# Performance work log

Measured on AMD Instinct MI355X. Metric: run time of the kernel, lower is better.

## Reference

```python
import jax, jax.numpy as jnp
import numpy as np
import math

E = 2048        # embed_dim
H = 16          # num_heads
HD = E // H // 2  # head_dim = 64
DEPTH = 12
LAMBDA_INIT = 0.8 - 0.6 * math.exp(-0.3 * DEPTH)


def setup_inputs() -> dict:
    key = jax.random.key(0)
    ks = jax.random.split(key, 9)
    s = 0.02
    return {
        "x": jax.random.normal(ks[0], (2, 2048, E), jnp.float32),
        "Wq": jax.random.normal(ks[1], (E, E), jnp.float32) * s,
        "Wk": jax.random.normal(ks[2], (E, E), jnp.float32) * s,  # n_rep = 1
        "Wv": jax.random.normal(ks[3], (E, E), jnp.float32) * s,
        "Wo": jax.random.normal(ks[4], (E, E), jnp.float32) * s,
        "lq1": jax.random.normal(ks[5], (HD,), jnp.float32) * 0.1,
        "lk1": jax.random.normal(ks[6], (HD,), jnp.float32) * 0.1,
        "lq2": jax.random.normal(ks[7], (HD,), jnp.float32) * 0.1,
        "lk2": jax.random.normal(ks[8], (HD,), jnp.float32) * 0.1,
    }


def reference(x, Wq, Wk, Wv, Wo, lq1, lk1, lq2, lk2):
    b, t, e = x.shape
    scaling = HD ** (-0.5)
    # projections; split into 2*H sub-heads of dim HD for q/k, H heads of 2*HD for v
    q = (x @ Wq).reshape(b, t, 2 * H, HD).transpose(0, 2, 1, 3) * scaling  # [b,2H,t,hd]
    k = (x @ Wk).reshape(b, t, 2 * H, HD).transpose(0, 2, 1, 3)           # [b,2H,t,hd]
    v = (x @ Wv).reshape(b, t, H, 2 * HD).transpose(0, 2, 1, 3)           # [b,H,t,2hd]

    scores = jnp.einsum('bhqd,bhkd->bhqk', q, k)  # [b,2H,t,t]
    causal = jnp.triu(jnp.full((t, t), -jnp.inf, dtype=jnp.float32), 1)
    aw = jax.nn.softmax((scores + causal).astype(jnp.float32), axis=-1)

    lam = (jnp.exp(jnp.sum(lq1 * lk1)) - jnp.exp(jnp.sum(lq2 * lk2)) + LAMBDA_INIT)
    aw = aw.reshape(b, H, 2, t, t)
    aw = aw[:, :, 0] - lam * aw[:, :, 1]  # differential attention

    attn = jnp.einsum('bhqk,bhkd->bhqd', aw, v)  # [b,H,t,2hd]
    # RMSNorm over last dim (no affine), eps=1e-5
    attn = attn * jax.lax.rsqrt(jnp.mean(attn * attn, axis=-1, keepdims=True) + 1e-5)
    attn = attn * (1.0 - LAMBDA_INIT)
    attn = attn.transpose(0, 2, 1, 3).reshape(b, t, H * 2 * HD)
    return attn @ Wo
```

## Files before the change

kernel.cpp:

```cpp
#include <hip/hip_runtime.h>
#include <stdint.h>

typedef __bf16 bf16_t;
typedef __bf16 bf16x8 __attribute__((ext_vector_type(8)));
typedef __bf16 bf16x4 __attribute__((ext_vector_type(4)));
typedef float  f32x4  __attribute__((ext_vector_type(4)));
typedef float  f32x16 __attribute__((ext_vector_type(16)));
typedef unsigned int u32;

#define L2E 1.44269504088896340736f
#define LAMBDA_INIT 0.7836057665316245f
#define ONE_MINUS_LAMBDA_INIT 0.2163942334683755f

__device__ __forceinline__ void gload_lds16(const void* g, void* l) {
  __builtin_amdgcn_global_load_lds(
      (const __attribute__((address_space(1))) char*)(uintptr_t)g,
      (__attribute__((address_space(3))) char*)(uintptr_t)l, 16, 0, 0);
}

__device__ __forceinline__ f32x4 mfma_bf16(bf16x8 a, bf16x8 b, f32x4 c) {
  return __builtin_amdgcn_mfma_f32_16x16x32_bf16(a, b, c, 0, 0, 0);
}
__device__ __forceinline__ f32x16 mfma32(bf16x8 a, bf16x8 b, f32x16 c) {
  return __builtin_amdgcn_mfma_f32_32x32x16_bf16(a, b, c, 0, 0, 0);
}

__device__ __forceinline__ u32 pkbf(float a, float b) {
  union { bf16_t h[2]; u32 u; } x;
  x.h[0] = (bf16_t)a; x.h[1] = (bf16_t)b;
  return x.u;
}
__device__ __forceinline__ void pl32swap(u32& a, u32& b) {
  asm volatile("v_permlane32_swap_b32 %0, %1" : "+v"(a), "+v"(b));
}

__global__ __launch_bounds__(256) void cvt_bf16(const float* __restrict__ in,
                                                bf16_t* __restrict__ out) {
  const size_t idx = ((size_t)blockIdx.x * 256 + threadIdx.x) * 8;
  float4 a = *(const float4*)(in + idx);
  float4 c = *(const float4*)(in + idx + 4);
  bf16x8 v;
  v[0] = (bf16_t)a.x; v[1] = (bf16_t)a.y; v[2] = (bf16_t)a.z; v[3] = (bf16_t)a.w;
  v[4] = (bf16_t)c.x; v[5] = (bf16_t)c.y; v[6] = (bf16_t)c.z; v[7] = (bf16_t)c.w;
  *(bf16x8*)(out + idx) = v;
}

struct WArgs {
  const float* W[4];
  bf16_t* WT[4];
  float sc[4];
};

__global__ __launch_bounds__(256) void cvt_wT_all(WArgs a) {
  __shared__ float t[64][65];
  const int i = blockIdx.z;
  const float* W = a.W[i];
  bf16_t* WT = a.WT[i];
  const float scale = a.sc[i];
  const int k0 = blockIdx.x * 64, n0 = blockIdx.y * 64;
  const int r = threadIdx.x >> 2, cg = threadIdx.x & 3;
#pragma unroll
  for (int q = 0; q < 4; ++q) {
    float4 v = *(const float4*)(W + (size_t)(k0 + r) * 2048 + n0 + cg * 16 + q * 4);
    t[r][cg * 16 + q * 4 + 0] = v.x;
    t[r][cg * 16 + q * 4 + 1] = v.y;
    t[r][cg * 16 + q * 4 + 2] = v.z;
    t[r][cg * 16 + q * 4 + 3] = v.w;
  }
  __syncthreads();
  bf16x8 o0, o1;
#pragma unroll
  for (int j = 0; j < 8; ++j) o0[j] = (bf16_t)(t[cg * 16 + j][r] * scale);
#pragma unroll
  for (int j = 0; j < 8; ++j) o1[j] = (bf16_t)(t[cg * 16 + 8 + j][r] * scale);
  bf16_t* dst = WT + (size_t)(n0 + r) * 2048 + k0 + cg * 16;
  *(bf16x8*)dst = o0;
  *(bf16x8*)(dst + 8) = o1;
}

__global__ void lam_kernel(const float* lq1, const float* lk1,
                           const float* lq2, const float* lk2, float* out) {
  const int l = threadIdx.x;
  float p1 = lq1[l] * lk1[l];
  float p2 = lq2[l] * lk2[l];
#pragma unroll
  for (int d = 1; d < 64; d <<= 1) {
    p1 += __shfl_xor(p1, d);
    p2 += __shfl_xor(p2, d);
  }
  if (l == 0) *out = expf(p1) - expf(p2) + LAMBDA_INIT;
}

__global__ __launch_bounds__(512, 2) void gemm256(const bf16_t* __restrict__ A,
                                                  const bf16_t* __restrict__ Bt,
                                                  bf16_t* __restrict__ Cqk) {
  extern __shared__ __align__(16) char sm[];
  const int tid = threadIdx.x;
  const int w = tid >> 6, lane = tid & 63;
  const int wr = w >> 2, wc = w & 3;
  const int lm = lane >> 4, ln = lane & 15;
  const int nwg = (int)(gridDim.x * gridDim.y);
  const int flat = (int)blockIdx.y * (int)gridDim.x + (int)blockIdx.x;
  const int swz = (flat & 7) * (nwg >> 3) + (flat >> 3);
  const int m0 = (swz & 15) * 256, n0 = (swz >> 4) * 256;

  int aoff[8], boff[4];
#pragma unroll
  for (int m = 0; m < 8; ++m) {
    const int row = wr * 128 + m * 16 + ln;
    aoff[m] = row * 64 + ((lm * 16) ^ ((((row >> 2) ^ row) & 3) << 4));
  }
#pragma unroll
  for (int n = 0; n < 4; ++n) {
    const int row = wc * 64 + n * 16 + ln;
    boff[n] = row * 64 + ((lm * 16) ^ ((((row >> 2) ^ row) & 3) << 4));
  }

  const bf16_t* gsrc[4];
  int ldst[4];
#pragma unroll
  for (int j = 0; j < 4; ++j) {
    const int r2 = j & 1, opB = j >> 1;
    const int row = r2 * 128 + w * 16 + (lane >> 2);
    const int colb = (lane & 3) * 16;
    const int cb = colb ^ ((((row >> 2) ^ row) & 3) << 4);
    gsrc[j] = (opB ? Bt + (size_t)(n0 + row) * 2048
                   : A + (size_t)(m0 + row) * 2048) + (cb >> 1);
    ldst[j] = opB * 16384 + r2 * 8192 + w * 1024;
  }

  const f32x4 vzero = {0.f, 0.f, 0.f, 0.f};
  f32x4 acc[8][4];
#pragma unroll
  for (int m = 0; m < 8; ++m)
#pragma unroll
    for (int n = 0; n < 4; ++n) acc[m][n] = vzero;

#pragma unroll
  for (int kt = 0; kt < 3; ++kt)
#pragma unroll
    for (int j = 0; j < 4; ++j)
      gload_lds16(gsrc[j] + kt * 32, sm + kt * 32768 + ldst[j]);
  asm volatile("s_waitcnt vmcnt(8)" ::: "memory");
  __builtin_amdgcn_s_barrier();

  for (int kt = 0; kt < 64; ++kt) {
    const char* sa = sm + (kt & 3) * 32768;
    const char* sb = sa + 16384;
    const int stage = kt + 3;
    char* sd = sm + (stage & 3) * 32768;
    bf16x8 bfr[4], af[4];

#pragma unroll
    for (int n = 0; n < 4; ++n) bfr[n] = *(const bf16x8*)(sb + boff[n]);
#pragma unroll
    for (int m = 0; m < 4; ++m) af[m] = *(const bf16x8*)(sa + aoff[m]);
    if (stage < 64) {
      gload_lds16(gsrc[0] + stage * 32, sd + ldst[0]);
      gload_lds16(gsrc[1] + stage * 32, sd + ldst[1]);
    }
    __builtin_amdgcn_s_barrier();
    __builtin_amdgcn_s_setprio(1);
#pragma unroll
    for (int m = 0; m < 4; ++m)
#pragma unroll
      for (int n = 0; n < 4; ++n) acc[m][n] = mfma_bf16(af[m], bfr[n], acc[m][n]);
    __builtin_amdgcn_s_setprio(0);
    __builtin_amdgcn_s_barrier();

#pragma unroll
    for (int m = 0; m < 4; ++m) af[m] = *(const bf16x8*)(sa + aoff[4 + m]);
    if (stage < 64) {
      gload_lds16(gsrc[2] + stage * 32, sd + ldst[2]);
      gload_lds16(gsrc[3] + stage * 32, sd + ldst[3]);
    }
    __builtin_amdgcn_s_barrier();
    __builtin_amdgcn_s_setprio(1);
#pragma unroll
    for (int m = 0; m < 4; ++m)
#pragma unroll
      for (int n = 0; n < 4; ++n)
        acc[4 + m][n] = mfma_bf16(af[m], bfr[n], acc[4 + m][n]);
    __builtin_amdgcn_s_setprio(0);
    if (kt < 61) {
      asm volatile("s_waitcnt vmcnt(8)" ::: "memory");
    } else if (kt == 61) {
      asm volatile("s_waitcnt vmcnt(4)" ::: "memory");
    } else if (kt == 62) {
      asm volatile("s_waitcnt vmcnt(0)" ::: "memory");
    }
    __builtin_amdgcn_s_barrier();
  }

  bf16_t* C = Cqk + (size_t)(n0 >> 11) * (4096u * 2048u);
#pragma unroll
  for (int m = 0; m < 8; ++m)
#pragma unroll
    for (int n = 0; n < 4; ++n)
#pragma unroll
      for (int r = 0; r < 4; ++r) {
        const size_t grow = m0 + wr * 128 + m * 16 + lm * 4 + r;
        const int gcol = (n0 + wc * 64 + n * 16 + ln) & 2047;
        C[grow * 2048 + gcol] = (bf16_t)acc[m][n][r];
      }
}

template <int OUTMODE>
__global__ __launch_bounds__(256, 2) void gemm_bt(const bf16_t* __restrict__ A,
                                                  const bf16_t* __restrict__ Bt,
                                                  void* __restrict__ Cv) {
  __shared__ __align__(16) bf16_t As[128 * 64];
  __shared__ __align__(16) bf16_t Bs[128 * 64];
  const int tid = threadIdx.x;
  const int w = tid >> 6, lane = tid & 63;
  const int wr = w >> 1, wc = w & 1;
  const int lm = lane >> 4, ln = lane & 15;
  const int nwg = (int)(gridDim.x * gridDim.y);
  const int flat = (int)blockIdx.y * (int)gridDim.x + (int)blockIdx.x;
  const int swz = (flat & 7) * (nwg >> 3) + (flat >> 3);
  const int m0 = (swz & 31) * 128, n0 = (swz >> 5) * 128;

  const f32x4 vzero = {0.f, 0.f, 0.f, 0.f};
  f32x4 acc[4][4];
#pragma unroll
  for (int m = 0; m < 4; ++m)
#pragma unroll
    for (int n = 0; n < 4; ++n) acc[m][n] = vzero;

  for (int k0 = 0; k0 < 2048; k0 += 64) {
    __syncthreads();
#pragma unroll
    for (int j = 0; j < 4; ++j) {
      const int inst = w * 4 + j;
      const int row = inst * 8 + (lane >> 3);
      const int cb = ((lane & 7) * 16) ^ ((row & 7) << 4);
      gload_lds16(A + (size_t)(m0 + row) * 2048 + k0 + (cb >> 1),
                  (char*)As + inst * 1024);
      gload_lds16(Bt + (size_t)(n0 + row) * 2048 + k0 + (cb >> 1),
                  (char*)Bs + inst * 1024);
    }
    asm volatile("s_waitcnt vmcnt(0)" ::: "memory");
    __syncthreads();

#pragma unroll
    for (int kc = 0; kc < 2; ++kc) {
      bf16x8 af[4], bfr[4];
#pragma unroll
      for (int m = 0; m < 4; ++m) {
        const int row = wr * 64 + m * 16 + ln;
        int off = row * 128 + kc * 64 + lm * 16;
        off ^= (row & 7) << 4;
        af[m] = *(const bf16x8*)((const char*)As + off);
      }
#pragma unroll
      for (int n = 0; n < 4; ++n) {
        const int row = wc * 64 + n * 16 + ln;
        int off = row * 128 + kc * 64 + lm * 16;
        off ^= (row & 7) << 4;
        bfr[n] = *(const bf16x8*)((const char*)Bs + off);
      }
      __builtin_amdgcn_s_setprio(1);
#pragma unroll
      for (int m = 0; m < 4; ++m)
#pragma unroll
        for (int n = 0; n < 4; ++n) acc[m][n] = mfma_bf16(af[m], bfr[n], acc[m][n]);
      __builtin_amdgcn_s_setprio(0);
    }
  }

  if (OUTMODE == 1) {
    bf16_t* C = (bf16_t*)Cv;
#pragma unroll
    for (int m = 0; m < 4; ++m) {
      const int growb = m0 + wr * 64 + m * 16 + lm * 4;
      const int bb = growb >> 11, t = growb & 2047;
      const int kt = t >> 6, kk = (t >> 4) & 3, hi2 = (t >> 3) & 1, e0 = t & 7;
#pragma unroll
      for (int n = 0; n < 4; ++n) {
        const int gcol = n0 + wc * 64 + n * 16 + ln;
        const int hh = gcol >> 7, g = (gcol >> 5) & 3, l31o = gcol & 31;
        bf16x4 v;
#pragma unroll
        for (int r = 0; r < 4; ++r) v[r] = (bf16_t)acc[m][n][r];
        const size_t idx = ((size_t)((bb * 16 + hh) * 32 + kt)) * 8192 +
                           (size_t)(((g * 4 + kk) * 64 + hi2 * 32 + l31o) * 8 + e0);
        *(bf16x4*)(C + idx) = v;
      }
    }
  } else {
    float* C = (float*)Cv;
#pragma unroll
    for (int m = 0; m < 4; ++m)
#pragma unroll
      for (int n = 0; n < 4; ++n)
#pragma unroll
        for (int r = 0; r < 4; ++r) {
          const size_t grow = m0 + wr * 64 + m * 16 + lm * 4 + r;
          const int gcol = n0 + wc * 64 + n * 16 + ln;
          C[grow * 2048 + gcol] = acc[m][n][r];
        }
  }
}

__global__ __launch_bounds__(256, 2) void flash_diff(const bf16_t* __restrict__ Q,
                                                     const bf16_t* __restrict__ K,
                                                     const bf16_t* __restrict__ Vf,
                                                     bf16_t* __restrict__ attnb,
                                                     const float* __restrict__ lamP) {
  __shared__ __align__(16) char smem[32768];

  const int tid = threadIdx.x;
  const int w = tid >> 6, lane = tid & 63;
  const int qh = w >> 1, s = w & 1;
  const int l31 = lane & 31, hi = lane >> 5;

  const int bid = (int)blockIdx.x;
  const int xcd = bid & 7, p = bid >> 3;
  const int qtp = p & 15, g2 = p >> 4;
  const int hb = g2 * 8 + xcd;
  const int h = hb & 15, b = hb >> 4;
  const size_t bt0 = (size_t)b * 2048;
  const float lam = *lamP;

  auto stage_k = [&](int buf, int k0) {
#pragma unroll
    for (int j = 0; j < 4; ++j) {
      const int inst = w * 4 + j;
      const int row = inst * 4 + (lane >> 4);
      const int cb = ((lane & 15) * 16) ^ ((row & 15) << 4);
      gload_lds16(K + (bt0 + k0 + row) * 2048 + h * 128 + (cb >> 1),
                  smem + buf * 16384 + inst * 1024);
    }
  };

  for (int half = 0; half < 2; ++half) {
    const int qt = half == 0 ? qtp : 31 - qtp;
    const int q0 = qt * 64;
    const int qloc = qh * 32 + l31;

    bf16x8 qf[4];
#pragma unroll
    for (int kc = 0; kc < 4; ++kc)
      qf[kc] = *(const bf16x8*)(Q + (bt0 + q0 + qloc) * 2048 + h * 128 +
                                s * 64 + kc * 16 + hi * 8);

    stage_k(0, 0);
    asm volatile("s_waitcnt vmcnt(0)" ::: "memory");
    __syncthreads();

    f32x16 accv[4];
#pragma unroll
    for (int m = 0; m < 4; ++m)
#pragma unroll
      for (int r = 0; r < 16; ++r) accv[m][r] = 0.f;
    float lsum = 0.f;

    int cur = 0;
    for (int kt = 0; kt <= qt; ++kt) {
      if (kt < qt) stage_k(cur ^ 1, (kt + 1) * 64);
      const char* Ksb = (const char*)smem + cur * 16384;

      const char* vsrc = (const char*)Vf +
                         (((size_t)((b * 16 + h) * 32 + kt)) << 14) + lane * 16;

      bf16x8 pf[2][2];
#pragma unroll
      for (int mt = 0; mt < 2; ++mt) {
        f32x16 sa;
#pragma unroll
        for (int r = 0; r < 16; ++r) sa[r] = 0.f;
        const int row = mt * 32 + l31;
        const int rswz = (row & 15) << 4;
        __builtin_amdgcn_s_setprio(1);
#pragma unroll
        for (int kc = 0; kc < 4; ++kc) {
          int off = row * 256 + s * 128 + kc * 32 + hi * 16;
          off ^= rswz;
          bf16x8 kf = *(const bf16x8*)(Ksb + off);
          sa = mfma32(kf, qf[kc], sa);
        }
        __builtin_amdgcn_s_setprio(0);

        if (kt == qt) {
#pragma unroll
          for (int r = 0; r < 16; ++r) {
            const int key = mt * 32 + (r & 3) + 8 * (r >> 2) + 4 * hi;
            if (key > qloc) sa[r] = -1e30f;
          }
        }
        float pv[16];
#pragma unroll
        for (int r = 0; r < 16; ++r) {
          pv[r] = exp2f(sa[r]);
          lsum += pv[r];
        }
        u32 c0 = pkbf(pv[0], pv[1]),   c1 = pkbf(pv[2], pv[3]);
        u32 c2 = pkbf(pv[4], pv[5]),   c3 = pkbf(pv[6], pv[7]);
        u32 c4 = pkbf(pv[8], pv[9]),   c5 = pkbf(pv[10], pv[11]);
        u32 c6 = pkbf(pv[12], pv[13]), c7 = pkbf(pv[14], pv[15]);
        pl32swap(c0, c2); pl32swap(c1, c3);
        pl32swap(c4, c6); pl32swap(c5, c7);
        union { u32 u[4]; bf16x8 v; } f0, f1;
        f0.u[0] = c0; f0.u[1] = c1; f0.u[2] = c2; f0.u[3] = c3;
        f1.u[0] = c4; f1.u[1] = c5; f1.u[2] = c6; f1.u[3] = c7;
        pf[mt][0] = f0.v;
        pf[mt][1] = f1.v;
      }

#pragma unroll
      for (int g = 0; g < 4; ++g) {
        bf16x8 vf[4];
#pragma unroll
        for (int kk = 0; kk < 4; ++kk)
          vf[kk] = *(const bf16x8*)(vsrc + (g * 4 + kk) * 1024);
        __builtin_amdgcn_s_setprio(1);
#pragma unroll
        for (int kk = 0; kk < 4; ++kk)
          accv[g] = mfma32(vf[kk], pf[kk >> 1][kk & 1], accv[g]);
        __builtin_amdgcn_s_setprio(0);
      }

      asm volatile("s_waitcnt vmcnt(0)" ::: "memory");
      __syncthreads();
      cur ^= 1;
    }

    lsum += __shfl_xor(lsum, 32);
    const float rl = 1.0f / lsum;
    float* Obuf = (float*)smem;

    if (s == 1) {
#pragma unroll
      for (int mt4 = 0; mt4 < 4; ++mt4)
#pragma unroll
        for (int q2 = 0; q2 < 4; ++q2) {
          f32x4 v;
#pragma unroll
          for (int e = 0; e < 4; ++e) v[e] = accv[mt4][q2 * 4 + e] * rl;
          const int d = mt4 * 32 + q2 * 8 + hi * 4;
          *(f32x4*)(Obuf + (size_t)qloc * 128 + d) = v;
        }
    }
    __syncthreads();
    if (s == 0) {
      float o[4][16];
      float ss = 0.f;
#pragma unroll
      for (int mt4 = 0; mt4 < 4; ++mt4)
#pragma unroll
        for (int q2 = 0; q2 < 4; ++q2) {
          const int d = mt4 * 32 + q2 * 8 + hi * 4;
          f32x4 ov = *(const f32x4*)(Obuf + (size_t)qloc * 128 + d);
#pragma unroll
          for (int e = 0; e < 4; ++e) {
            const float v = accv[mt4][q2 * 4 + e] * rl - lam * ov[e];
            o[mt4][q2 * 4 + e] = v;
            ss += v * v;
          }
        }
      ss += __shfl_xor(ss, 32);
      const float sc = rsqrtf(ss * (1.0f / 128.f) + 1e-5f) * ONE_MINUS_LAMBDA_INIT;
      const size_t grow = bt0 + q0 + qloc;
#pragma unroll
      for (int mt4 = 0; mt4 < 4; ++mt4)
#pragma unroll
        for (int q2 = 0; q2 < 4; ++q2) {
          const int d = mt4 * 32 + q2 * 8 + hi * 4;
          bf16x4 v;
#pragma unroll
          for (int e = 0; e < 4; ++e) v[e] = (bf16_t)(o[mt4][q2 * 4 + e] * sc);
          *(bf16x4*)(attnb + grow * 2048 + h * 128 + d) = v;
        }
    }
    __syncthreads();
  }
}

extern "C" void kernel_launch(void* const* d_in, const int* in_sizes, int n_in,
                              void* d_out, int out_size, void* d_ws, size_t ws_size,
                              hipStream_t stream) {
  const float* x   = (const float*)d_in[0];
  const float* Wq  = (const float*)d_in[1];
  const float* Wk  = (const float*)d_in[2];
  const float* Wv  = (const float*)d_in[3];
  const float* Wo  = (const float*)d_in[4];
  const float* lq1 = (const float*)d_in[5];
  const float* lk1 = (const float*)d_in[6];
  const float* lq2 = (const float*)d_in[7];
  const float* lk2 = (const float*)d_in[8];

  char* ws = (char*)d_ws;
  bf16_t* xb    = (bf16_t*)(ws + 0);
  bf16_t* wqT   = (bf16_t*)(ws + 16777216);
  bf16_t* wvT   = (bf16_t*)(ws + 33554432);
  bf16_t* woT   = (bf16_t*)(ws + 41943040);
  bf16_t* Qb    = (bf16_t*)(ws + 50331648);
  bf16_t* Kb    = (bf16_t*)(ws + 67108864);
  bf16_t* Vfb   = (bf16_t*)(ws + 16777216);
  bf16_t* attnb = (bf16_t*)(ws + 0);
  float*  lamP  = (float*)(ws + 83886080);

  hipFuncSetAttribute((const void*)gemm256,
                      hipFuncAttributeMaxDynamicSharedMemorySize, 131072);

  cvt_bf16<<<4096, 256, 0, stream>>>(x, xb);
  WArgs wa;
  wa.W[0] = Wq; wa.W[1] = Wk; wa.W[2] = Wv; wa.W[3] = Wo;
  wa.WT[0] = wqT; wa.WT[1] = wqT + 4194304; wa.WT[2] = wvT; wa.WT[3] = woT;
  wa.sc[0] = 0.125f * L2E; wa.sc[1] = 1.0f; wa.sc[2] = 1.0f; wa.sc[3] = 1.0f;
  cvt_wT_all<<<dim3(32, 32, 4), 256, 0, stream>>>(wa);
  lam_kernel<<<1, 64, 0, stream>>>(lq1, lk1, lq2, lk2, lamP);

  gemm256<<<dim3(16, 16), 512, 131072, stream>>>(xb, wqT, Qb);
  gemm_bt<1><<<dim3(32, 16), 256, 0, stream>>>(xb, wvT, (void*)Vfb);

  flash_diff<<<512, 256, 0, stream>>>(Qb, Kb, Vfb, attnb, lamP);

  gemm_bt<2><<<dim3(32, 16), 256, 0, stream>>>(attnb, woT, d_out);
}
```

Before: 272.4 us.

## Split flash attention KV loop across two wave groups with LDS merge

Doubles the flash_diff block to 512 threads and has two wave groups process the even and odd key tiles in parallel. Each group stages its own K tiles into separate LDS halves, and partial accumulators and row sums are merged through shared memory before the differential combine and RMSNorm. This shortens the serial KV loop per block to raise parallelism in the causal attention. In exchange it doubles LDS to 64KB and adds an extra reduction pass with syncs, which may lower occupancy, and waves with no tile on short rows sit idle.

```diff
diff --git a/kernel.cpp b/kernel.cpp
--- a/kernel.cpp
+++ b/kernel.cpp
@@ -302,16 +302,18 @@
   }
 }
 
-__global__ __launch_bounds__(256, 2) void flash_diff(const bf16_t* __restrict__ Q,
+__global__ __launch_bounds__(512, 2) void flash_diff(const bf16_t* __restrict__ Q,
                                                      const bf16_t* __restrict__ K,
                                                      const bf16_t* __restrict__ Vf,
                                                      bf16_t* __restrict__ attnb,
                                                      const float* __restrict__ lamP) {
-  __shared__ __align__(16) char smem[32768];
+  __shared__ __align__(16) char smem[65536];
+  __shared__ float lsumb[2][64];
 
   const int tid = threadIdx.x;
   const int w = tid >> 6, lane = tid & 63;
-  const int qh = w >> 1, s = w & 1;
+  const int kh = w & 1, s = (w >> 1) & 1, qh = w >> 2;
+  const int wg = w >> 1;
   const int l31 = lane & 31, hi = lane >> 5;
 
   const int bid = (int)blockIdx.x;
@@ -322,14 +324,19 @@
   const size_t bt0 = (size_t)b * 2048;
   const float lam = *lamP;
 
+  f32x16 vz16;
+#pragma unroll
+  for (int r = 0; r < 16; ++r) vz16[r] = 0.f;
+  asm volatile("" : "+v"(vz16));
+
   auto stage_k = [&](int buf, int k0) {
 #pragma unroll
     for (int j = 0; j < 4; ++j) {
-      const int inst = w * 4 + j;
+      const int inst = wg * 4 + j;
       const int row = inst * 4 + (lane >> 4);
       const int cb = ((lane & 15) * 16) ^ ((row & 15) << 4);
       gload_lds16(K + (bt0 + k0 + row) * 2048 + h * 128 + (cb >> 1),
-                  smem + buf * 16384 + inst * 1024);
+                  smem + kh * 32768 + buf * 16384 + inst * 1024);
     }
   };
 
@@ -344,80 +351,81 @@
       qf[kc] = *(const bf16x8*)(Q + (bt0 + q0 + qloc) * 2048 + h * 128 +
                                 s * 64 + kc * 16 + hi * 8);
 
-    stage_k(0, 0);
+    if (kh <= qt) stage_k(0, kh * 64);
     asm volatile("s_waitcnt vmcnt(0)" ::: "memory");
     __syncthreads();
 
     f32x16 accv[4];
 #pragma unroll
-    for (int m = 0; m < 4; ++m)
-#pragma unroll
-      for (int r = 0; r < 16; ++r) accv[m][r] = 0.f;
+    for (int m = 0; m < 4; ++m) accv[m] = vz16;
     float lsum = 0.f;
 
+    const int R = (qt >> 1) + 1;
     int cur = 0;
-    for (int kt = 0; kt <= qt; ++kt) {
-      if (kt < qt) stage_k(cur ^ 1, (kt + 1) * 64);
-      const char* Ksb = (const char*)smem + cur * 16384;
-
-      const char* vsrc = (const char*)Vf +
-                         (((size_t)((b * 16 + h) * 32 + kt)) << 14) + lane * 16;
-
-      bf16x8 pf[2][2];
-#pragma unroll
-      for (int mt = 0; mt < 2; ++mt) {
-        f32x16 sa;
-#pragma unroll
-        for (int r = 0; r < 16; ++r) sa[r] = 0.f;
-        const int row = mt * 32 + l31;
-        const int rswz = (row & 15) << 4;
-        __builtin_amdgcn_s_setprio(1);
-#pragma unroll
-        for (int kc = 0; kc < 4; ++kc) {
-          int off = row * 256 + s * 128 + kc * 32 + hi * 16;
-          off ^= rswz;
-          bf16x8 kf = *(const bf16x8*)(Ksb + off);
-          sa = mfma32(kf, qf[kc], sa);
-        }
-        __builtin_amdgcn_s_setprio(0);
-
-        if (kt == qt) {
-#pragma unroll
-          for (int r = 0; r < 16; ++r) {
-            const int key = mt * 32 + (r & 3) + 8 * (r >> 2) + 4 * hi;
-            if (key > qloc) sa[r] = -1e30f;
+    for (int r = 0; r < R; ++r) {
+      const int kt = 2 * r + kh;
+      const bool active = kt <= qt;
+      if (active && kt + 2 <= qt) stage_k(cur ^ 1, (kt + 2) * 64);
+
+      if (active) {
+        const char* Ksb = (const char*)smem + kh * 32768 + cur * 16384;
+        const char* vsrc = (const char*)Vf +
+                           (((size_t)((b * 16 + h) * 32 + kt)) << 14) + lane * 16;
+
+        bf16x8 pf[2][2];
+#pragma unroll
+        for (int mt = 0; mt < 2; ++mt) {
+          const int row = mt * 32 + l31;
+          const int rswz = (row & 15) << 4;
+          f32x16 sa;
+          __builtin_amdgcn_s_setprio(1);
+#pragma unroll
+          for (int kc = 0; kc < 4; ++kc) {
+            int off = row * 256 + s * 128 + kc * 32 + hi * 16;
+            off ^= rswz;
+            bf16x8 kf = *(const bf16x8*)(Ksb + off);
+            sa = mfma32(kf, qf[kc], kc == 0 ? vz16 : sa);
           }
-        }
-        float pv[16];
-#pragma unroll
-        for (int r = 0; r < 16; ++r) {
-          pv[r] = exp2f(sa[r]);
-          lsum += pv[r];
-        }
-        u32 c0 = pkbf(pv[0], pv[1]),   c1 = pkbf(pv[2], pv[3]);
-        u32 c2 = pkbf(pv[4], pv[5]),   c3 = pkbf(pv[6], pv[7]);
-        u32 c4 = pkbf(pv[8], pv[9]),   c5 = pkbf(pv[10], pv[11]);
-        u32 c6 = pkbf(pv[12], pv[13]), c7 = pkbf(pv[14], pv[15]);
-        pl32swap(c0, c2); pl32swap(c1, c3);
-        pl32swap(c4, c6); pl32swap(c5, c7);
-        union { u32 u[4]; bf16x8 v; } f0, f1;
-        f0.u[0] = c0; f0.u[1] = c1; f0.u[2] = c2; f0.u[3] = c3;
-        f1.u[0] = c4; f1.u[1] = c5; f1.u[2] = c6; f1.u[3] = c7;
-        pf[mt][0] = f0.v;
-        pf[mt][1] = f1.v;
-      }
-
-#pragma unroll
-      for (int g = 0; g < 4; ++g) {
-        bf16x8 vf[4];
-#pragma unroll
-        for (int kk = 0; kk < 4; ++kk)
-          vf[kk] = *(const bf16x8*)(vsrc + (g * 4 + kk) * 1024);
-        __builtin_amdgcn_s_setprio(1);
-#pragma unroll
-        for (int kk = 0; kk < 4; ++kk)
-          accv[g] = mfma32(vf[kk], pf[kk >> 1][kk & 1], accv[g]);
-        __builtin_amdgcn_s_setprio(0);
+          __builtin_amdgcn_s_setprio(0);
+
+          if (kt == qt) {
+#pragma unroll
+            for (int r2 = 0; r2 < 16; ++r2) {
+              const int key = mt * 32 + (r2 & 3) + 8 * (r2 >> 2) + 4 * hi;
+              if (key > qloc) sa[r2] = -1e30f;
+            }
+          }
+          float pv[16];
+#pragma unroll
+          for (int r2 = 0; r2 < 16; ++r2) {
+            pv[r2] = exp2f(sa[r2]);
+            lsum += pv[r2];
+          }
+          u32 c0 = pkbf(pv[0], pv[1]),   c1 = pkbf(pv[2], pv[3]);
+          u32 c2 = pkbf(pv[4], pv[5]),   c3 = pkbf(pv[6], pv[7]);
+          u32 c4 = pkbf(pv[8], pv[9]),   c5 = pkbf(pv[10], pv[11]);
+          u32 c6 = pkbf(pv[12], pv[13]), c7 = pkbf(pv[14], pv[15]);
+          pl32swap(c0, c2); pl32swap(c1, c3);
+          pl32swap(c4, c6); pl32swap(c5, c7);
+          union { u32 u[4]; bf16x8 v; } f0, f1;
+          f0.u[0] = c0; f0.u[1] = c1; f0.u[2] = c2; f0.u[3] = c3;
+          f1.u[0] = c4; f1.u[1] = c5; f1.u[2] = c6; f1.u[3] = c7;
+          pf[mt][0] = f0.v;
+          pf[mt][1] = f1.v;
+        }
+
+#pragma unroll
+        for (int g = 0; g < 4; ++g) {
+          bf16x8 vf[4];
+#pragma unroll
+          for (int kk = 0; kk < 4; ++kk)
+            vf[kk] = *(const bf16x8*)(vsrc + (g * 4 + kk) * 1024);
+          __builtin_amdgcn_s_setprio(1);
+#pragma unroll
+          for (int kk = 0; kk < 4; ++kk)
+            accv[g] = mfma32(vf[kk], pf[kk >> 1][kk & 1], accv[g]);
+          __builtin_amdgcn_s_setprio(0);
+        }
       }
 
       asm volatile("s_waitcnt vmcnt(0)" ::: "memory");
@@ -426,10 +434,40 @@
     }
 
     lsum += __shfl_xor(lsum, 32);
-    const float rl = 1.0f / lsum;
+
+    if (kh == 1) {
+      if (hi == 0) lsumb[s][qh * 32 + l31] = lsum;
+      float* dst = (float*)(smem + (s * 2 + qh) * 16384) + l31 * 128;
+#pragma unroll
+      for (int mt4 = 0; mt4 < 4; ++mt4)
+#pragma unroll
+        for (int q2 = 0; q2 < 4; ++q2) {
+          f32x4 v;
+#pragma unroll
+          for (int e = 0; e < 4; ++e) v[e] = accv[mt4][q2 * 4 + e];
+          *(f32x4*)(dst + mt4 * 32 + q2 * 8 + hi * 4) = v;
+        }
+    }
+    __syncthreads();
+
+    float rl = 0.f;
+    if (kh == 0) {
+      lsum += lsumb[s][qh * 32 + l31];
+      rl = 1.0f / lsum;
+      const float* src = (const float*)(smem + (s * 2 + qh) * 16384) + l31 * 128;
+#pragma unroll
+      for (int mt4 = 0; mt4 < 4; ++mt4)
+#pragma unroll
+        for (int q2 = 0; q2 < 4; ++q2) {
+          f32x4 v = *(const f32x4*)(src + mt4 * 32 + q2 * 8 + hi * 4);
+#pragma unroll
+          for (int e = 0; e < 4; ++e) accv[mt4][q2 * 4 + e] += v[e];
+        }
+    }
+    __syncthreads();
+
     float* Obuf = (float*)smem;
-
-    if (s == 1) {
+    if (kh == 0 && s == 1) {
 #pragma unroll
       for (int mt4 = 0; mt4 < 4; ++mt4)
 #pragma unroll
@@ -442,7 +480,7 @@
         }
     }
     __syncthreads();
-    if (s == 0) {
+    if (kh == 0 && s == 0) {
       float o[4][16];
       float ss = 0.f;
 #pragma unroll
@@ -514,7 +552,7 @@
   gemm256<<<dim3(16, 16), 512, 131072, stream>>>(xb, wqT, Qb);
   gemm_bt<1><<<dim3(32, 16), 256, 0, stream>>>(xb, wvT, (void*)Vfb);
 
-  flash_diff<<<512, 256, 0, stream>>>(Qb, Kb, Vfb, attnb, lamP);
+  flash_diff<<<512, 512, 0, stream>>>(Qb, Kb, Vfb, attnb, lamP);
 
   gemm_bt<2><<<dim3(32, 16), 256, 0, stream>>>(attnb, woT, d_out);
 }
```

Result: slower. 293.4 us (+7.7%).
